# Kernel tuning notes

Hardware: AMD Instinct MI355X
Metric: run time of the kernel (lower is better)

## Reference

```python
import jax, jax.numpy as jnp
import numpy as np

B, N, IN_DIM, OUT_DIM, HEADS = 4, 1024, 128, 128, 8
D = OUT_DIM // HEADS  # per-head dim = 16


def setup_inputs() -> dict:
    key = jax.random.key(0)
    k1, k2, k3, k4 = jax.random.split(key, 4)
    x = jax.random.normal(k1, (B, N, IN_DIM), dtype=jnp.float32)
    adj = jax.random.randint(k2, (B, N, N), 0, 2).astype(jnp.float32)
    W = jax.random.normal(k3, (IN_DIM, OUT_DIM), dtype=jnp.float32) * (IN_DIM ** -0.5)
    a = jax.random.normal(k4, (2 * D, 1), dtype=jnp.float32) * ((2 * D) ** -0.5)
    return {"x": x, "adj": adj, "W": W, "a": a}


def reference(x, adj, W, a):
    Bv, Nv, _ = x.shape
    # adj = clamp(adj + I, 0, 1); used only as a 0/1 mask
    mask = jnp.clip(adj + jnp.eye(Nv, dtype=adj.dtype)[None], 0.0, 1.0) > 0  # (B,N,N)
    xt = (x @ W).reshape(Bv, Nv, HEADS, D)  # (B,N,H,D)
    # a([x_i, x_j]) == x_i @ a_src + x_j @ a_dst  (exact decomposition of concat+linear)
    a_src, a_dst = a[:D, 0], a[D:, 0]
    src = jnp.einsum('bnhd,d->bnh', xt, a_src)
    dst = jnp.einsum('bnhd,d->bnh', xt, a_dst)
    e = jax.nn.leaky_relu(src[:, :, None, :] + dst[:, None, :, :], negative_slope=0.2)  # (B,i,j,H)
    m = mask[..., None]  # (B,N,N,1) broadcast over heads
    neg_inf = jnp.asarray(-jnp.inf, e.dtype)
    # max over neighbors j (dim=2), detached, diagonal guarantees >=1 valid entry
    mx = jax.lax.stop_gradient(jnp.max(jnp.where(m, e, neg_inf), axis=2, keepdims=True))
    # Faithful to torch code: masked entries become 0 (NOT -inf) before softmax,
    # so they contribute exp(0)=1 to the softmax, exactly as in the original.
    e_stable = jnp.where(m, e - mx, jnp.zeros((), e.dtype))
    alpha = jax.nn.softmax(e_stable, axis=2)  # (B,i,j,H)
    h = jnp.einsum('bijh,bjhd->bihd', alpha, xt).reshape(Bv, Nv, HEADS * D)  # concat=True
    return jax.nn.relu(h)
```

## Files before the change

### kernel.cpp

```cpp
#include <hip/hip_runtime.h>
#include <hip/hip_bf16.h>
#include <math.h>
#include <stdint.h>

#define BV 4
#define NV 1024
#define IND 128
#define OUTD 128
#define NH 8
#define DD 16
#define LOG2E 1.4426950408889634f

typedef __attribute__((ext_vector_type(8))) short bf16x8;
typedef __attribute__((ext_vector_type(4))) float f32x4;

__device__ __forceinline__ ushort bf16rne(float f) {
    uint32_t u = __float_as_uint(f);
    u += 0x7fff + ((u >> 16) & 1);
    return (ushort)(u >> 16);
}

__device__ __forceinline__ uint32_t cvtpk_bf16(float lo, float hi) {
    uint32_t r;
    asm("v_cvt_pk_bf16_f32 %0, %1, %2" : "=v"(r) : "v"(lo), "v"(hi));
    return r;
}

__device__ __forceinline__ float vexp2(float x) {
    float r;
    asm("v_exp_f32 %0, %1" : "=v"(r) : "v"(x));
    return r;
}

__global__ __launch_bounds__(256) void kA(
    const float* __restrict__ x, const float* __restrict__ adj,
    const float* __restrict__ W, const float* __restrict__ a,
    uint32_t* __restrict__ bits, ushort* __restrict__ xhi,
    float* __restrict__ src, float* __restrict__ dst_t)
{
    const int pid = blockIdx.x;
    const int tid = threadIdx.x;

    if (pid >= 512) {
        const int row = pid - 512;
        const int i = row & (NV - 1);
        const int wave = tid >> 6, lane = tid & 63;
        const float* arow = adj + (size_t)row * NV;
        #pragma unroll
        for (int r = 0; r < 4; ++r) {
            const int j = (r * 4 + wave) * 64 + lane;
            const bool m = (arow[j] > 0.f) || (j == i);
            const unsigned long long bal = __ballot(m);
            if (lane == 0) {
                bits[(size_t)row * 32 + (r * 4 + wave) * 2]     = (uint32_t)bal;
                bits[(size_t)row * 32 + (r * 4 + wave) * 2 + 1] = (uint32_t)(bal >> 32);
            }
        }
        return;
    }

    const int jt = pid & 15, bh = pid >> 4;
    const int b = bh >> 3, h = bh & 7;
    const int j0 = jt * 64;
    const int jl = tid >> 2, dq = tid & 3;
    const int gj = b * NV + j0 + jl;

    float acc0 = 0.f, acc1 = 0.f, acc2 = 0.f, acc3 = 0.f;
    const float* xrow = x + (size_t)gj * IND;
    const float* wcol = W + h * DD + dq * 4;

    #pragma unroll
    for (int kc = 0; kc < IND; kc += 32) {
        float4 xr[8];
        #pragma unroll
        for (int u = 0; u < 8; ++u)
            xr[u] = *(const float4*)&xrow[kc + u * 4];
        #pragma unroll
        for (int u = 0; u < 8; ++u) {
            #pragma unroll
            for (int v = 0; v < 4; ++v) {
                const float xs = ((const float*)&xr[u])[v];
                const float4 w = *(const float4*)&wcol[(size_t)(kc + u * 4 + v) * OUTD];
                acc0 = fmaf(xs, w.x, acc0);
                acc1 = fmaf(xs, w.y, acc1);
                acc2 = fmaf(xs, w.z, acc2);
                acc3 = fmaf(xs, w.w, acc3);
            }
        }
    }

    {
        const int d0 = dq * 4;
        float s = acc0 * a[d0] + acc1 * a[d0 + 1] + acc2 * a[d0 + 2] + acc3 * a[d0 + 3];
        float t = acc0 * a[DD + d0] + acc1 * a[DD + d0 + 1] + acc2 * a[DD + d0 + 2] + acc3 * a[DD + d0 + 3];
        s += __shfl_xor(s, 1); s += __shfl_xor(s, 2);
        t += __shfl_xor(t, 1); t += __shfl_xor(t, 2);
        if (dq == 0) {
            src[(size_t)gj * NH + h] = s * LOG2E;
            dst_t[(size_t)bh * NV + j0 + jl] = t * LOG2E;
        }
    }

    __shared__ ushort thi[16][80];
    {
        const float av[4] = {acc0, acc1, acc2, acc3};
        #pragma unroll
        for (int i2 = 0; i2 < 4; ++i2)
            thi[dq * 4 + i2][jl] = bf16rne(av[i2]);
    }
    __syncthreads();
    if (tid < 128) {
        const int d = tid >> 3, jo = tid & 7;
        const uint4 vh = *(const uint4*)&thi[d][jo * 8];
        const size_t base = ((size_t)(bh * 16 + d)) * NV + j0 + jo * 8;
        *(uint4*)&xhi[base] = vh;
    }
}

__global__ __launch_bounds__(256, 6) void kB(
    const uint32_t* __restrict__ bits, const ushort* __restrict__ xhi,
    const float* __restrict__ dst_t, const float* __restrict__ src,
    float* __restrict__ out)
{
    const int bid = blockIdx.x;
    const int xcd = bid & 7, t2 = (bid >> 3) & 3, it = bid >> 5;
    const int bh = xcd * 4 + t2;
    const int b = bh >> 3, h = bh & 7;
    const int i0 = it * 16;

    const int tid = threadIdx.x;
    const int jq = tid >> 6, lane = tid & 63;
    const int g = lane >> 4, r16 = lane & 15;

    __shared__ float dstl[NV];
    __shared__ float mxr[4][16];
    __shared__ float red_acc[3][64][4];
    __shared__ float red_den[3][64];

    {
        const float4* gd = (const float4*)(dst_t + (size_t)bh * NV);
        *(float4*)&dstl[tid * 4] = gd[tid];
    }
    const int grow = b * NV + i0 + r16;
    const float srcv = src[(size_t)grow * NH + h];
    uint32_t blw[8];
    #pragma unroll
    for (int s = 0; s < 8; ++s)
        blw[s] = bits[(size_t)grow * 32 + jq * 8 + s];
    __syncthreads();

    float dmax = -INFINITY;
    #pragma unroll
    for (int s = 0; s < 8; ++s) {
        const int base = jq * 256 + s * 32 + g * 8;
        const uint32_t bb = (blw[s] >> (g * 8)) & 0xffu;
        const float4 v0 = *(const float4*)&dstl[base];
        const float4 v1 = *(const float4*)&dstl[base + 4];
        const float dv[8] = {v0.x, v0.y, v0.z, v0.w, v1.x, v1.y, v1.z, v1.w};
        #pragma unroll
        for (int t = 0; t < 8; t += 2) {
            const float s0 = (bb & (1u << t)) ? dv[t] : -INFINITY;
            const float s1 = (bb & (1u << (t + 1))) ? dv[t + 1] : -INFINITY;
            dmax = fmaxf(dmax, fmaxf(s0, s1));
        }
    }
    dmax = fmaxf(dmax, __shfl_xor(dmax, 16));
    dmax = fmaxf(dmax, __shfl_xor(dmax, 32));
    if (g == 0) mxr[jq][r16] = dmax;
    __syncthreads();
    dmax = fmaxf(fmaxf(mxr[0][r16], mxr[1][r16]), fmaxf(mxr[2][r16], mxr[3][r16]));
    const float S = srcv + dmax;
    const float mxv = fmaxf(S, 0.2f * S);

    const float Ac = srcv - mxv;
    const float Bc = fmaf(0.2f, srcv, -mxv);
    f32x4 acc = {0.f, 0.f, 0.f, 0.f};
    float den0 = 0.f, den1 = 0.f;
    const ushort* xrow = xhi + ((size_t)(bh * 16 + r16)) * NV;
    #pragma unroll
    for (int s = 0; s < 8; ++s) {
        const int base = jq * 256 + s * 32 + g * 8;
        const uint32_t bb = (blw[s] >> (g * 8)) & 0xffu;
        const float4 v0 = *(const float4*)&dstl[base];
        const float4 v1 = *(const float4*)&dstl[base + 4];
        const float dv[8] = {v0.x, v0.y, v0.z, v0.w, v1.x, v1.y, v1.z, v1.w};
        float w[8];
        #pragma unroll
        for (int t = 0; t < 8; ++t) {
            const float arg = fmaxf(dv[t] + Ac, fmaf(0.2f, dv[t], Bc));
            const float argsel = (bb & (1u << t)) ? arg : 0.0f;
            w[t] = vexp2(argsel);
        }
        den0 += (w[0] + w[2]) + (w[4] + w[6]);
        den1 += (w[1] + w[3]) + (w[5] + w[7]);
        union { uint32_t u[4]; bf16x8 v; } af;
        af.u[0] = cvtpk_bf16(w[0], w[1]);
        af.u[1] = cvtpk_bf16(w[2], w[3]);
        af.u[2] = cvtpk_bf16(w[4], w[5]);
        af.u[3] = cvtpk_bf16(w[6], w[7]);
        const bf16x8 vh = *(const bf16x8*)&xrow[base];
        acc = __builtin_amdgcn_mfma_f32_16x16x32_bf16(af.v, vh, acc, 0, 0, 0);
    }
    float den = den0 + den1;

    if (jq > 0) {
        *(float4*)&red_acc[jq - 1][lane][0] = *(float4*)&acc;
        red_den[jq - 1][lane] = den;
    }
    __syncthreads();
    if (jq == 0) {
        #pragma unroll
        for (int qq = 0; qq < 3; ++qq) {
            const float4 oa = *(const float4*)&red_acc[qq][lane][0];
            acc[0] += oa.x; acc[1] += oa.y; acc[2] += oa.z; acc[3] += oa.w;
            den += red_den[qq][lane];
        }
        den += __shfl_xor(den, 16);
        den += __shfl_xor(den, 32);
        #pragma unroll
        for (int q = 0; q < 4; ++q) {
            const int orow = g * 4 + q;
            const float dq = __shfl(den, orow);
            float rv = acc[q] / dq;
            rv = fmaxf(rv, 0.f);
            out[((size_t)(b * NV) + i0 + orow) * OUTD + h * 16 + r16] = rv;
        }
    }
}

extern "C" void kernel_launch(void* const* d_in, const int* in_sizes, int n_in,
                              void* d_out, int out_size, void* d_ws, size_t ws_size,
                              hipStream_t stream)
{
    const float* x   = (const float*)d_in[0];
    const float* adj = (const float*)d_in[1];
    const float* W   = (const float*)d_in[2];
    const float* a   = (const float*)d_in[3];
    float* out = (float*)d_out;

    char* ws = (char*)d_ws;
    ushort* xhi    = (ushort*)ws;
    float* dst_t   = (float*)(ws + 1024 * 1024);
    float* src     = (float*)(ws + 1024 * 1024 + 128 * 1024);
    uint32_t* bits = (uint32_t*)(ws + 1024 * 1024 + 256 * 1024);

    kA<<<512 + BV * NV, 256, 0, stream>>>(x, adj, W, a, bits, xhi, src, dst_t);
    kB<<<2048, 256, 0, stream>>>(bits, xhi, dst_t, src, out);
}
```

Baseline: 30.99 us.

## Replace per-row masked max pass with global upper bound and rescaled masked-entry term

Drops the first pass over the neighbour list that computed each row's masked maximum, along with its shared-memory reduction and barrier. Exponents are now shifted by a per-row upper bound built from the global dst maximum. The reference's per-row masked max is still tracked alongside the single pass and used afterwards to add the masked-out entries' contribution exactly. That contribution goes through a second MFMA against a mask-complement indicator plus a count of masked bits. Launch bounds also rise from 6 to 8 blocks per CU. The cost is one extra MFMA and extra packing per step, more registers under a tighter occupancy target, and possible exp underflow when the bound sits far above the true row max.

```diff
diff --git a/kernel.cpp b/kernel.cpp
--- a/kernel.cpp
+++ b/kernel.cpp
@@ -117,7 +117,7 @@
     }
 }
 
-__global__ __launch_bounds__(256, 6) void kB(
+__global__ __launch_bounds__(256, 8) void kB(
     const uint32_t* __restrict__ bits, const ushort* __restrict__ xhi,
     const float* __restrict__ dst_t, const float* __restrict__ src,
     float* __restrict__ out)
@@ -133,13 +133,19 @@
     const int g = lane >> 4, r16 = lane & 15;
 
     __shared__ float dstl[NV];
-    __shared__ float mxr[4][16];
-    __shared__ float red_acc[3][64][4];
-    __shared__ float red_den[3][64];
-
+    __shared__ float gmx[4];
+    __shared__ float red[3][64][12];
+
+    float wmax;
     {
         const float4* gd = (const float4*)(dst_t + (size_t)bh * NV);
-        *(float4*)&dstl[tid * 4] = gd[tid];
+        const float4 v = gd[tid];
+        *(float4*)&dstl[tid * 4] = v;
+        wmax = fmaxf(fmaxf(v.x, v.y), fmaxf(v.z, v.w));
+        #pragma unroll
+        for (int o = 1; o < 64; o <<= 1)
+            wmax = fmaxf(wmax, __shfl_xor(wmax, o));
+        if (lane == 0) gmx[jq] = wmax;
     }
     const int grow = b * NV + i0 + r16;
     const float srcv = src[(size_t)grow * NH + h];
@@ -149,79 +155,83 @@
         blw[s] = bits[(size_t)grow * 32 + jq * 8 + s];
     __syncthreads();
 
-    float dmax = -INFINITY;
-    #pragma unroll
-    for (int s = 0; s < 8; ++s) {
-        const int base = jq * 256 + s * 32 + g * 8;
-        const uint32_t bb = (blw[s] >> (g * 8)) & 0xffu;
-        const float4 v0 = *(const float4*)&dstl[base];
-        const float4 v1 = *(const float4*)&dstl[base + 4];
-        const float dv[8] = {v0.x, v0.y, v0.z, v0.w, v1.x, v1.y, v1.z, v1.w};
-        #pragma unroll
-        for (int t = 0; t < 8; t += 2) {
-            const float s0 = (bb & (1u << t)) ? dv[t] : -INFINITY;
-            const float s1 = (bb & (1u << (t + 1))) ? dv[t + 1] : -INFINITY;
-            dmax = fmaxf(dmax, fmaxf(s0, s1));
-        }
-    }
-    dmax = fmaxf(dmax, __shfl_xor(dmax, 16));
-    dmax = fmaxf(dmax, __shfl_xor(dmax, 32));
-    if (g == 0) mxr[jq][r16] = dmax;
-    __syncthreads();
-    dmax = fmaxf(fmaxf(mxr[0][r16], mxr[1][r16]), fmaxf(mxr[2][r16], mxr[3][r16]));
-    const float S = srcv + dmax;
-    const float mxv = fmaxf(S, 0.2f * S);
-
-    const float Ac = srcv - mxv;
-    const float Bc = fmaf(0.2f, srcv, -mxv);
-    f32x4 acc = {0.f, 0.f, 0.f, 0.f};
-    float den0 = 0.f, den1 = 0.f;
+    const float gdmax = fmaxf(fmaxf(gmx[0], gmx[1]), fmaxf(gmx[2], gmx[3]));
+    const float Scu = srcv + gdmax;
+    const float Cub = fmaxf(Scu, 0.2f * Scu);
+    const float Ac = srcv - Cub;
+    const float Bc = fmaf(0.2f, srcv, -Cub);
+
+    f32x4 acc  = {0.f, 0.f, 0.f, 0.f};
+    f32x4 accu = {0.f, 0.f, 0.f, 0.f};
+    float den = 0.f, dmaxarg = -INFINITY;
+    int nmask = 0;
     const ushort* xrow = xhi + ((size_t)(bh * 16 + r16)) * NV;
     #pragma unroll
     for (int s = 0; s < 8; ++s) {
         const int base = jq * 256 + s * 32 + g * 8;
         const uint32_t bb = (blw[s] >> (g * 8)) & 0xffu;
+        nmask += __popc(bb);
         const float4 v0 = *(const float4*)&dstl[base];
         const float4 v1 = *(const float4*)&dstl[base + 4];
         const float dv[8] = {v0.x, v0.y, v0.z, v0.w, v1.x, v1.y, v1.z, v1.w};
-        float w[8];
+        float wm[8];
         #pragma unroll
         for (int t = 0; t < 8; ++t) {
             const float arg = fmaxf(dv[t] + Ac, fmaf(0.2f, dv[t], Bc));
-            const float argsel = (bb & (1u << t)) ? arg : 0.0f;
-            w[t] = vexp2(argsel);
-        }
-        den0 += (w[0] + w[2]) + (w[4] + w[6]);
-        den1 += (w[1] + w[3]) + (w[5] + w[7]);
-        union { uint32_t u[4]; bf16x8 v; } af;
-        af.u[0] = cvtpk_bf16(w[0], w[1]);
-        af.u[1] = cvtpk_bf16(w[2], w[3]);
-        af.u[2] = cvtpk_bf16(w[4], w[5]);
-        af.u[3] = cvtpk_bf16(w[6], w[7]);
+            const float ex = vexp2(arg);
+            const bool mbit = (bb >> t) & 1u;
+            wm[t] = mbit ? ex : 0.0f;
+            dmaxarg = fmaxf(dmaxarg, mbit ? arg : -INFINITY);
+        }
+        den += ((wm[0] + wm[1]) + (wm[2] + wm[3])) + ((wm[4] + wm[5]) + (wm[6] + wm[7]));
+        union { uint32_t u[4]; bf16x8 v; } af, afi;
+        #pragma unroll
+        for (int p = 0; p < 4; ++p) {
+            af.u[p] = cvtpk_bf16(wm[2 * p], wm[2 * p + 1]);
+            const float i0f = ((bb >> (2 * p)) & 1u) ? 0.0f : 1.0f;
+            const float i1f = ((bb >> (2 * p + 1)) & 1u) ? 0.0f : 1.0f;
+            afi.u[p] = cvtpk_bf16(i0f, i1f);
+        }
         const bf16x8 vh = *(const bf16x8*)&xrow[base];
-        acc = __builtin_amdgcn_mfma_f32_16x16x32_bf16(af.v, vh, acc, 0, 0, 0);
-    }
-    float den = den0 + den1;
+        acc  = __builtin_amdgcn_mfma_f32_16x16x32_bf16(af.v,  vh, acc, 0, 0, 0);
+        accu = __builtin_amdgcn_mfma_f32_16x16x32_bf16(afi.v, vh, accu, 0, 0, 0);
+    }
 
     if (jq > 0) {
-        *(float4*)&red_acc[jq - 1][lane][0] = *(float4*)&acc;
-        red_den[jq - 1][lane] = den;
+        float* rp = &red[jq - 1][lane][0];
+        *(float4*)&rp[0] = *(float4*)&acc;
+        *(float4*)&rp[4] = *(float4*)&accu;
+        rp[8] = den;
+        rp[9] = dmaxarg;
+        rp[10] = (float)nmask;
     }
     __syncthreads();
     if (jq == 0) {
+        float fnm = (float)nmask;
         #pragma unroll
         for (int qq = 0; qq < 3; ++qq) {
-            const float4 oa = *(const float4*)&red_acc[qq][lane][0];
-            acc[0] += oa.x; acc[1] += oa.y; acc[2] += oa.z; acc[3] += oa.w;
-            den += red_den[qq][lane];
-        }
-        den += __shfl_xor(den, 16);
-        den += __shfl_xor(den, 32);
+            const float* rp = &red[qq][lane][0];
+            const float4 oa = *(const float4*)&rp[0];
+            const float4 ou = *(const float4*)&rp[4];
+            acc[0] += oa.x;  acc[1] += oa.y;  acc[2] += oa.z;  acc[3] += oa.w;
+            accu[0] += ou.x; accu[1] += ou.y; accu[2] += ou.z; accu[3] += ou.w;
+            den += rp[8];
+            dmaxarg = fmaxf(dmaxarg, rp[9]);
+            fnm += rp[10];
+        }
+        den += __shfl_xor(den, 16);  den += __shfl_xor(den, 32);
+        fnm += __shfl_xor(fnm, 16);  fnm += __shfl_xor(fnm, 32);
+        dmaxarg = fmaxf(dmaxarg, __shfl_xor(dmaxarg, 16));
+        dmaxarg = fmaxf(dmaxarg, __shfl_xor(dmaxarg, 32));
+        const float K = vexp2(dmaxarg);
+        const float dfull = fmaf(K, 1024.0f - fnm, den);
         #pragma unroll
         for (int q = 0; q < 4; ++q) {
             const int orow = g * 4 + q;
-            const float dq = __shfl(den, orow);
-            float rv = acc[q] / dq;
+            const float kq = __shfl(K, orow);
+            const float dq = __shfl(dfull, orow);
+            const float num = fmaf(kq, accu[q], acc[q]);
+            float rv = num / dq;
             rv = fmaxf(rv, 0.f);
             out[((size_t)(b * NV) + i0 + orow) * OUTD + h * 16 + r16] = rv;
         }
```

New measurement: 33.26 us. 7.3% more time.
